# Kernel optimization log

Hardware: AMD Instinct MI355X
Metric: run time of the kernel (lower is better)

The kernel has to match this reference:

```python
import jax, jax.numpy as jnp
import numpy as np

# EKV constants from Config
VT = 0.025
N_FACTOR = 1.5
VD = 0.5
ALPHA = 2e-06
BASE_TIA = 500000.0

KERNEL = 3
STRIDE = 1
PAD = 1


def _unfold(x, k, stride, pad):
    # torch.nn.functional.unfold: (N, C, H, W) -> (N, C*k*k, L), patch dims ordered (c, kh, kw)
    N, C, H, W = x.shape
    xp = jnp.pad(x, ((0, 0), (0, 0), (pad, pad), (pad, pad)))
    Ho = (H + 2 * pad - k) // stride + 1
    Wo = (W + 2 * pad - k) // stride + 1
    patches = []
    for i in range(k):
        for j in range(k):
            patches.append(xp[:, :, i:i + stride * Ho:stride, j:j + stride * Wo:stride])
    # (k*k, N, C, Ho, Wo) -> (N, C, k*k, Ho*Wo) -> (N, C*k*k, L)
    p = jnp.stack(patches, axis=2)  # (N, C, k*k, Ho, Wo)
    return p.reshape(N, C * k * k, Ho * Wo), Ho, Wo


def setup_inputs() -> dict:
    key = jax.random.key(0)
    k1, k2 = jax.random.split(key)
    x = jax.random.normal(k1, (4, 64, 32, 32), dtype=jnp.float32)
    # theta ~ Normal(2.5, 0.5), shape (out_channels, in_channels, k, k)
    theta = 2.5 + 0.5 * jax.random.normal(k2, (64, 64, 3, 3), dtype=jnp.float32)
    return {"x": x, "theta": theta}


def reference(x, theta):
    N, C, H, W = x.shape
    O = theta.shape[0]
    fan_in = C * KERNEL * KERNEL
    tia_gain = BASE_TIA / (fan_in ** 0.5)
    phi = 2 * N_FACTOR * VT

    x_unf, Ho, Wo = _unfold(x, KERNEL, STRIDE, PAD)      # (N, C*k*k, L)
    x_in = x_unf[:, None, :, :]                           # (N, 1, CKK, L)
    w_th = theta.reshape(1, O, -1, 1)                     # (1, O, CKK, 1)

    v_diff = x_in - w_th                                  # (N, O, CKK, L)
    f_term = jnp.square(jax.nn.softplus(v_diff / phi))
    r_term = jnp.square(jax.nn.softplus((v_diff - VD) / phi))
    i_syn = ALPHA * (f_term - r_term)
    out_current = jnp.sum(i_syn, axis=2)                  # (N, O, L)
    out_voltage = out_current * tia_gain
    return out_voltage.reshape(N, O, Ho, Wo)
```

## Files before the change

### kernel.cpp

```cpp
#include <hip/hip_runtime.h>
#include <math.h>

#define HH 32
#define WW 32
#define CIN 64
#define NO 64
#define NCK 576
#define X_ELEMS 262144
#define NP2 8192
#define STRIDE_E 296

#define WS_W    0
#define WS_TAU  36864
#define WS_N    37504
#define WS_LC   45696
#define WS_LX   (WS_LC + NP2 * STRIDE_E)

__device__ __forceinline__ float fexp2(float x) {
#if __has_builtin(__builtin_amdgcn_exp2f)
    return __builtin_amdgcn_exp2f(x);
#else
    return exp2f(x);
#endif
}
__device__ __forceinline__ float flog2(float x) {
#if __has_builtin(__builtin_amdgcn_logf)
    return __builtin_amdgcn_logf(x);
#else
    return log2f(x);
#endif
}

__global__ __launch_bounds__(256) void prep_kernel(const float* __restrict__ theta,
                                                   float* __restrict__ ws) {
    constexpr float SZ = 19.235933878519512f;
    const int b = blockIdx.x, t = threadIdx.x;
    if (b < 144) {
        int i = b * 256 + t;
        int o = i & 63, ck = i >> 6;
        float th = theta[o * NCK + ck];
        ws[WS_W + i] = -SZ * th;
        float mn = th;
#pragma unroll
        for (int s = 32; s > 0; s >>= 1)
            mn = fminf(mn, __shfl_xor(mn, s, 64));
        if (o == 0) ws[WS_TAU + ck] = SZ * mn - 8.0f;
    } else {
        if (t < 64) ws[WS_TAU + NCK + t] = 1e30f;
    }
}

__global__ __launch_bounds__(512) void build_kernel(const float* __restrict__ x,
                                                    float* __restrict__ ws) {
    constexpr float SZ = 19.235933878519512f;
    const int t    = threadIdx.x;
    const int lane = t & 63;
    const int wv   = __builtin_amdgcn_readfirstlane(t >> 6);
    const int p2   = (int)blockIdx.x * 8 + wv;
    const int pix  = p2 >> 1, half = p2 & 1;
    const int n  = pix >> 10;
    const int ho = (pix >> 5) & 31;
    const int wo = pix & 31;
    const int c0 = half * 32;

    int l = lane;
    int c_off = l / 9; if (c_off > 6) c_off = 6;
    int k = l - 9 * c_off; if (k > 8) k = 8;
    int di = k / 3, dj = k - 3 * (k / 3);
    int h = ho + di - 1, w_ = wo + dj - 1;
    bool sval = (h >= 0) && (h < HH) && (w_ >= 0) && (w_ < WW);
    int hc = min(max(h, 0), HH - 1), wc = min(max(w_, 0), WW - 1);
    float msc = ((l < 63) && sval) ? SZ : 0.0f;

    int gidx = n * (CIN * HH * WW) + (c0 + c_off) * 1024 + hc * WW + wc;
    const float* tw = ws + WS_TAU + c0 * 9;

    int*   listC = (int*)ws + WS_LC + p2 * STRIDE_E;
    float* listX = ws + WS_LX + p2 * STRIDE_E;
    int cnt = 0;

    float xv = x[min(gidx, X_ELEMS - 1)];
    float tv = tw[l];

    for (int cb = 0; cb < 32; cb += 7) {
        int cc = 32 - cb; if (cc > 7) cc = 7;
        int gidx2 = gidx + 7 * 1024;
        const float* tw2 = tw + 63;
        float xvn = xv, tvn = tv;
        if (cb + 7 < 32) { xvn = x[min(gidx2, X_ELEMS - 1)]; tvn = tw2[l]; }

        float xs = xv * msc;
        bool a = (xs >= tv) && (l < cc * 9);
        unsigned long long act = __ballot(a);
        unsigned lo32 = (unsigned)act, hi32 = (unsigned)(act >> 32);
        int idx = __builtin_amdgcn_mbcnt_hi(hi32,
                      __builtin_amdgcn_mbcnt_lo(lo32, 0));
        if (a) {
            listC[cnt + idx] = (c0 + cb) * 9 + l;
            listX[cnt + idx] = xs;
        }
        cnt += __popcll(act);
        gidx = gidx2; tw = tw2; xv = xvn; tv = tvn;
    }
    int padn = (-cnt) & 3;
    if (lane < padn) { listC[cnt + lane] = 0; listX[cnt + lane] = -100000.0f; }
    cnt += padn;
    if (lane == 0) ((int*)ws)[WS_N + p2] = cnt >> 2;
}

__global__ __launch_bounds__(512) void ekv_kernel(
        const float* __restrict__ ws, float* __restrict__ out) {
    constexpr float C2 = 1.2726342e-3f;
    constexpr float OS = 0.020018875579925058f;

    __shared__ float part[4][64];

    const int t    = threadIdx.x;
    const int lane = t & 63;
    const int wv   = __builtin_amdgcn_readfirstlane(t >> 6);
    const int p2   = (int)blockIdx.x * 8 + wv;
    const int pix  = p2 >> 1, half = p2 & 1;
    const int px   = wv >> 1;
    const int n  = pix >> 10;
    const int ho = (pix >> 5) & 31;
    const int wo = pix & 31;

    const int rounds = ((const int*)ws)[WS_N + p2];
    const int4*   LC = (const int4*)((const int*)ws + WS_LC + p2 * STRIDE_E);
    const float4* LX = (const float4*)(ws + WS_LX + p2 * STRIDE_E);
    const float* wsW = ws + WS_W;

    float accF = 0.f, accR = 0.f;

#define EKV_BODY(SX, WV)                                                   \
    {                                                                      \
        float z  = (WV) + (SX);                        \
        float e  = fexp2(z);                                               \
        float f  = flog2(1.0f + e);                                        \
        float rr = flog2(fmaf(C2, e, 1.0f));                               \
        accF = fmaf(f, f, accF);                                           \
        accR = fmaf(rr, rr, accR);                                         \
    }

    if (rounds > 0) {
        int4   cq = LC[0];
        float4 xq = LX[0];
        for (int r = 0; r < rounds; ++r) {
            int4 cqn = cq; float4 xqn = xq;
            if (r + 1 < rounds) { cqn = LC[r + 1]; xqn = LX[r + 1]; }
            float W0 = wsW[(cq.x << 6) + lane];
            float W1 = wsW[(cq.y << 6) + lane];
            float W2 = wsW[(cq.z << 6) + lane];
            float W3 = wsW[(cq.w << 6) + lane];
            EKV_BODY(xq.x, W0)
            EKV_BODY(xq.y, W1)
            EKV_BODY(xq.z, W2)
            EKV_BODY(xq.w, W3)
            cq = cqn; xq = xqn;
        }
    }
#undef EKV_BODY

    float p = accF - accR;
    if (half == 1) part[px][lane] = p;
    __syncthreads();
    if (half == 0)
        out[((n * NO + lane) * HH + ho) * WW + wo] = (p + part[px][lane]) * OS;
}

extern "C" void kernel_launch(void* const* d_in, const int* in_sizes, int n_in,
                              void* d_out, int out_size, void* d_ws, size_t ws_size,
                              hipStream_t stream) {
    const float* x     = (const float*)d_in[0];
    const float* theta = (const float*)d_in[1];
    float* out = (float*)d_out;
    float* ws  = (float*)d_ws;

    prep_kernel <<<145, 256, 0, stream>>>(theta, ws);
    build_kernel<<<1024, 512, 0, stream>>>(x, ws);
    ekv_kernel  <<<1024, 512, 0, stream>>>(ws, out);
}
```

Measured before the change: 78.22 us.

## Fuse active-list build into EKV kernel using shared memory lists

Merges the build and EKV kernels so each wavefront compacts its active (channel, tap) list into LDS rather than global workspace, then consumes it directly. This drops one kernel launch and the global write and read of the per-pixel lists and counts. It adds about 19 KB of LDS per block, which may lower occupancy. The list stride shrinks to 292 entries while staying a multiple of 4, so the int4/float4 LDS reads stay aligned.

```diff
diff --git a/kernel.cpp b/kernel.cpp
--- a/kernel.cpp
+++ b/kernel.cpp
@@ -7,14 +7,10 @@
 #define NO 64
 #define NCK 576
 #define X_ELEMS 262144
-#define NP2 8192
-#define STRIDE_E 296
+#define STRIDE_E 292
 
 #define WS_W    0
 #define WS_TAU  36864
-#define WS_N    37504
-#define WS_LC   45696
-#define WS_LX   (WS_LC + NP2 * STRIDE_E)
 
 __device__ __forceinline__ float fexp2(float x) {
 #if __has_builtin(__builtin_amdgcn_exp2f)
@@ -50,14 +46,23 @@
     }
 }
 
-__global__ __launch_bounds__(512) void build_kernel(const float* __restrict__ x,
-                                                    float* __restrict__ ws) {
+__global__ __launch_bounds__(512) void ekv_kernel(
+        const float* __restrict__ x, const float* __restrict__ ws,
+        float* __restrict__ out) {
     constexpr float SZ = 19.235933878519512f;
+    constexpr float C2 = 1.2726342e-3f;
+    constexpr float OS = 0.020018875579925058f;
+
+    __shared__ int   lc[8][STRIDE_E];
+    __shared__ float lx[8][STRIDE_E];
+    __shared__ float part[4][64];
+
     const int t    = threadIdx.x;
     const int lane = t & 63;
     const int wv   = __builtin_amdgcn_readfirstlane(t >> 6);
     const int p2   = (int)blockIdx.x * 8 + wv;
     const int pix  = p2 >> 1, half = p2 & 1;
+    const int px   = wv >> 1;
     const int n  = pix >> 10;
     const int ho = (pix >> 5) & 31;
     const int wo = pix & 31;
@@ -75,10 +80,7 @@
     int gidx = n * (CIN * HH * WW) + (c0 + c_off) * 1024 + hc * WW + wc;
     const float* tw = ws + WS_TAU + c0 * 9;
 
-    int*   listC = (int*)ws + WS_LC + p2 * STRIDE_E;
-    float* listX = ws + WS_LX + p2 * STRIDE_E;
     int cnt = 0;
-
     float xv = x[min(gidx, X_ELEMS - 1)];
     float tv = tw[l];
 
@@ -96,38 +98,18 @@
         int idx = __builtin_amdgcn_mbcnt_hi(hi32,
                       __builtin_amdgcn_mbcnt_lo(lo32, 0));
         if (a) {
-            listC[cnt + idx] = (c0 + cb) * 9 + l;
-            listX[cnt + idx] = xs;
+            lc[wv][cnt + idx] = (c0 + cb) * 9 + l;
+            lx[wv][cnt + idx] = xs;
         }
-        cnt += __popcll(act);
+        cnt += (int)__popcll(act);
         gidx = gidx2; tw = tw2; xv = xvn; tv = tvn;
     }
     int padn = (-cnt) & 3;
-    if (lane < padn) { listC[cnt + lane] = 0; listX[cnt + lane] = -100000.0f; }
-    cnt += padn;
-    if (lane == 0) ((int*)ws)[WS_N + p2] = cnt >> 2;
-}
+    if (lane < padn) { lc[wv][cnt + lane] = 0; lx[wv][cnt + lane] = -100000.0f; }
+    const int rounds = (cnt + padn) >> 2;
 
-__global__ __launch_bounds__(512) void ekv_kernel(
-        const float* __restrict__ ws, float* __restrict__ out) {
-    constexpr float C2 = 1.2726342e-3f;
-    constexpr float OS = 0.020018875579925058f;
-
-    __shared__ float part[4][64];
-
-    const int t    = threadIdx.x;
-    const int lane = t & 63;
-    const int wv   = __builtin_amdgcn_readfirstlane(t >> 6);
-    const int p2   = (int)blockIdx.x * 8 + wv;
-    const int pix  = p2 >> 1, half = p2 & 1;
-    const int px   = wv >> 1;
-    const int n  = pix >> 10;
-    const int ho = (pix >> 5) & 31;
-    const int wo = pix & 31;
-
-    const int rounds = ((const int*)ws)[WS_N + p2];
-    const int4*   LC = (const int4*)((const int*)ws + WS_LC + p2 * STRIDE_E);
-    const float4* LX = (const float4*)(ws + WS_LX + p2 * STRIDE_E);
+    const int4*   LC = (const int4*)&lc[wv][0];
+    const float4* LX = (const float4*)&lx[wv][0];
     const float* wsW = ws + WS_W;
 
     float accF = 0.f, accR = 0.f;
@@ -176,7 +158,6 @@
     float* out = (float*)d_out;
     float* ws  = (float*)d_ws;
 
-    prep_kernel <<<145, 256, 0, stream>>>(theta, ws);
-    build_kernel<<<1024, 512, 0, stream>>>(x, ws);
-    ekv_kernel  <<<1024, 512, 0, stream>>>(ws, out);
+    prep_kernel<<<145, 256, 0, stream>>>(theta, ws);
+    ekv_kernel <<<1024, 512, 0, stream>>>(x, ws, out);
 }
```

New measurement: 72.46 us. -7.4%, faster.
